# Kernel optimization log

Hardware: AMD Instinct MI355X
Metric: run time of the kernel (lower is better)

## Reference

```python
import jax, jax.numpy as jnp
import numpy as np

EPS = 0.1  # FAConv default eps


def setup_inputs() -> dict:
    key = jax.random.key(0)
    k1, k2, k3, k4, k5 = jax.random.split(key, 5)
    N, D, E, Dout = 50000, 128, 600000, 128
    x = jax.random.normal(k1, (N, D), dtype=jnp.float32)
    edge_index = jax.random.randint(k2, (2, E), 0, N, dtype=jnp.int64)
    # glorot-style scale for att vectors (Linear(D,1)) and weight matrix
    att_l = jax.random.normal(k3, (D,), dtype=jnp.float32) * (1.0 / np.sqrt(D))
    att_r = jax.random.normal(k4, (D,), dtype=jnp.float32) * (1.0 / np.sqrt(D))
    weight = jax.random.normal(k5, (D, Dout), dtype=jnp.float32) * np.sqrt(6.0 / (D + Dout))
    bias = jnp.zeros((Dout,), dtype=jnp.float32)
    return {"x": x, "edge_index": edge_index, "att_l": att_l, "att_r": att_r,
            "weight": weight, "bias": bias}


def reference(x, edge_index, att_l, att_r, weight, bias):
    N, D = x.shape
    # gcn_norm with add_self_loops=True
    loops = jnp.arange(N, dtype=edge_index.dtype)
    row = jnp.concatenate([edge_index[0], loops])  # source nodes
    col = jnp.concatenate([edge_index[1], loops])  # target nodes
    deg = jax.ops.segment_sum(jnp.ones_like(col, dtype=x.dtype), col, num_segments=N)
    dinv = jnp.where(deg > 0, jax.lax.rsqrt(jnp.maximum(deg, 1e-12)), 0.0)
    norm = dinv[row] * dinv[col]  # [E+N]
    # FAConv attention: alpha = tanh(att_l . x_j + att_r . x_i)
    al = x @ att_l  # [N]
    ar = x @ att_r  # [N]
    a = jnp.tanh(al[row] + ar[col])  # per-edge
    msg = x[row] * (a * norm)[:, None]  # [E+N, D]
    agg = jax.ops.segment_sum(msg, col, num_segments=N)
    h = agg + EPS * x  # x_0 == x in SAGNN.forward
    return h @ weight + bias
```

## Files before the change

kernel.cpp:

```cpp
#include <hip/hip_runtime.h>
#include <hip/hip_bf16.h>

#define FA_EPS 0.1f
#define BUCKET_M 48

typedef _Float16 half8  __attribute__((ext_vector_type(8)));
typedef float    f32x4  __attribute__((ext_vector_type(4)));

__device__ __forceinline__ float fast_tanh(float x) {
    float z = __builtin_amdgcn_exp2f(x * 2.885390081777927f);
    return 1.f - 2.f * __builtin_amdgcn_rcpf(z + 1.f);
}


__global__ __launch_bounds__(256) void k_node_prep(
    const float* __restrict__ x,
    const float* __restrict__ att_l,
    const float* __restrict__ att_r,
    const float* __restrict__ w,
    uint4* __restrict__ R,
    unsigned char* __restrict__ x8,
    _Float16* __restrict__ wt, int N)
{
    int gtid = (int)(blockIdx.x * blockDim.x + threadIdx.x);
    if (gtid < 128 * 128) {
        int k = gtid >> 7, n = gtid & 127;
        wt[n * 128 + k] = (_Float16)w[k * 128 + n];
    }
    int wave = gtid >> 6;
    int lane = threadIdx.x & 63;
    int half = lane >> 5;
    int sl   = lane & 31;
    int node = wave * 2 + half;
    if (node >= N) return;
    float4 v  = ((const float4*)(x + (size_t)node * 128))[sl];
    float4 l4 = ((const float4*)att_l)[sl];
    float4 r4 = ((const float4*)att_r)[sl];
    float pal = v.x * l4.x + v.y * l4.y + v.z * l4.z + v.w * l4.w;
    float par = v.x * r4.x + v.y * r4.y + v.z * r4.z + v.w * r4.w;
    float pm  = fmaxf(fmaxf(fabsf(v.x), fabsf(v.y)),
                      fmaxf(fabsf(v.z), fabsf(v.w)));
    #pragma unroll
    for (int off = 16; off > 0; off >>= 1) {
        pal += __shfl_xor(pal, off);
        par += __shfl_xor(par, off);
        pm   = fmaxf(pm, __shfl_xor(pm, off));
    }
    float rs = pm > 1e-20f ? 127.f / pm : 0.f;
    unsigned int q0 = (unsigned int)(int)rintf(fmaf(v.x, rs, 128.f));
    unsigned int q1 = (unsigned int)(int)rintf(fmaf(v.y, rs, 128.f));
    unsigned int q2 = (unsigned int)(int)rintf(fmaf(v.z, rs, 128.f));
    unsigned int q3 = (unsigned int)(int)rintf(fmaf(v.w, rs, 128.f));
    q0 = q0 > 255u ? 255u : q0;  q1 = q1 > 255u ? 255u : q1;
    q2 = q2 > 255u ? 255u : q2;  q3 = q3 > 255u ? 255u : q3;
    ((unsigned int*)(x8 + (size_t)node * 128))[sl] =
        q0 | (q1 << 8) | (q2 << 16) | (q3 << 24);
    if (sl == 0)
        R[node] = make_uint4(0u, __float_as_uint(pal),
                             __float_as_uint(pm * (1.f / 127.f)),
                             __float_as_uint(par));
}

__global__ __launch_bounds__(256) void k_edge(
    const int* __restrict__ ei,
    uint4* __restrict__ R,
    unsigned int* __restrict__ csr, int E)
{
    int e = (int)(blockIdx.x * blockDim.x + threadIdx.x);
    if (e >= E) return;
    int s = ei[e];
    int t = ei[E + e];
    unsigned int pos = atomicAdd((unsigned int*)(R + t), 1u);
    if (pos < BUCKET_M)
        csr[(size_t)t * BUCKET_M + pos] = (unsigned int)s;
}

__global__ __launch_bounds__(256) void k_gather(
    const unsigned char* __restrict__ x8,
    const unsigned int* __restrict__ csr,
    const uint4* __restrict__ R,
    _Float16* __restrict__ h16, int N)
{
    int wave = (int)((blockIdx.x * blockDim.x + threadIdx.x) >> 6);
    int lane = threadIdx.x & 63;
    int g  = lane >> 4;
    int sl = lane & 15;
    int t  = wave * 4 + g;
    bool valid = t < N;
    int tc = valid ? t : N - 1;
    uint4 rt = R[tc];
    unsigned int dt = rt.x;
    float al_t = __uint_as_float(rt.y);
    float s_t  = __uint_as_float(rt.z);
    float ar_t = __uint_as_float(rt.w);
    unsigned int cnt = dt < BUCKET_M ? dt : BUCKET_M;
    if (!valid) cnt = 0u;
    float dinv_t = __builtin_amdgcn_rsqf((float)(dt + 1u));
    const unsigned int* cs = csr + (size_t)tc * BUCKET_M;
    float acc[8];
    #pragma unroll
    for (int c = 0; c < 8; ++c) acc[c] = 0.f;
    float accB = 0.f;
    int gbase = lane & 0x30;
    for (unsigned int j0 = 0; j0 < cnt; j0 += 16) {
        unsigned int nb = cnt - j0; if (nb > 16u) nb = 16u;
        unsigned int myidx = j0 + (unsigned int)sl;
        bool own = myidx < cnt;
        unsigned int em = cs[own ? myidx : cnt - 1u];
        uint4 rsm = R[em];
        float am = own ? fast_tanh(__uint_as_float(rsm.y) + ar_t)
                         * __builtin_amdgcn_rsqf((float)(rsm.x + 1u))
                         * __uint_as_float(rsm.z)
                       : 0.f;
        const uint4* bp = (const uint4*)(cs + j0);
        uint4 b0 = bp[0], b1 = bp[1], b2 = bp[2], b3 = bp[3];
        unsigned int eu[16];
        eu[0]=b0.x;  eu[1]=b0.y;  eu[2]=b0.z;  eu[3]=b0.w;
        eu[4]=b1.x;  eu[5]=b1.y;  eu[6]=b1.z;  eu[7]=b1.w;
        eu[8]=b2.x;  eu[9]=b2.y;  eu[10]=b2.z; eu[11]=b2.w;
        eu[12]=b3.x; eu[13]=b3.y; eu[14]=b3.z; eu[15]=b3.w;
        uint2 d[16];
        #pragma unroll
        for (int u = 0; u < 16; ++u) {
            unsigned int e = (u < (int)nb) ? eu[u] : 0u;
            d[u] = *(const uint2*)(x8 + (size_t)e * 128 + sl * 8);
        }
        #pragma unroll
        for (int u = 0; u < 16; ++u) {
            float a = __shfl(am, gbase + u);
            accB += a;
            unsigned int lo = d[u].x, hi = d[u].y;
            acc[0] += a * (float)( lo        & 0xffu);
            acc[1] += a * (float)((lo >>  8) & 0xffu);
            acc[2] += a * (float)((lo >> 16) & 0xffu);
            acc[3] += a * (float)( lo >> 24        );
            acc[4] += a * (float)( hi        & 0xffu);
            acc[5] += a * (float)((hi >>  8) & 0xffu);
            acc[6] += a * (float)((hi >> 16) & 0xffu);
            acc[7] += a * (float)( hi >> 24        );
        }
    }
    float selfc  = fast_tanh(al_t + ar_t) * dinv_t * dinv_t + FA_EPS;
    float selfAs = selfc * s_t;
    float K = -128.f * fmaf(accB, dinv_t, selfAs);
    uint2 dself = *(const uint2*)(x8 + (size_t)tc * 128 + sl * 8);
    float bt[8];
    bt[0] = (float)( dself.x        & 0xffu);
    bt[1] = (float)((dself.x >>  8) & 0xffu);
    bt[2] = (float)((dself.x >> 16) & 0xffu);
    bt[3] = (float)( dself.x >> 24        );
    bt[4] = (float)( dself.y        & 0xffu);
    bt[5] = (float)((dself.y >>  8) & 0xffu);
    bt[6] = (float)((dself.y >> 16) & 0xffu);
    bt[7] = (float)( dself.y >> 24        );
    if (valid) {
        half8 hv;
        #pragma unroll
        for (int c = 0; c < 8; ++c)
            hv[c] = (_Float16)fmaf(acc[c], dinv_t, fmaf(selfAs, bt[c], K));
        *((half8*)(h16 + (size_t)t * 128) + sl) = hv;
    }
}

__global__ __launch_bounds__(256) void k_matmul_mfma(
    const _Float16* __restrict__ h16,
    const _Float16* __restrict__ wt,
    const float* __restrict__ bias,
    float* __restrict__ out, int N)
{
    __shared__ _Float16 wl[128 * 136];
    int tid = threadIdx.x;
    {
        const float* wsrc = (const float*)wt;
        float* wdst = (float*)wl;
        #pragma unroll
        for (int i = tid; i < 8192; i += 256)
            wdst[(i >> 6) * 68 + (i & 63)] = wsrc[i];
    }
    __syncthreads();
    int wv   = tid >> 6;
    int lane = tid & 63;
    int m    = lane & 15;
    int quad = lane >> 4;
    int r0 = (int)blockIdx.x * 64 + wv * 16;
    f32x4 acc[8];
    #pragma unroll
    for (int t = 0; t < 8; ++t) acc[t] = (f32x4)0.f;
    const _Float16* arow = h16 + (size_t)(r0 + m) * 128 + quad * 8;
    #pragma unroll
    for (int k0 = 0; k0 < 128; k0 += 32) {
        half8 a = *(const half8*)(arow + k0);
        #pragma unroll
        for (int t = 0; t < 8; ++t) {
            const _Float16* bp = wl + (size_t)(t * 16 + m) * 136 + quad * 8 + k0;
            half8 b = *(const half8*)bp;
            acc[t] = __builtin_amdgcn_mfma_f32_16x16x32_f16(a, b, acc[t], 0, 0, 0);
        }
    }
    int orow = r0 + quad * 4;
    #pragma unroll
    for (int t = 0; t < 8; ++t) {
        int col = t * 16 + m;
        float bc = bias[col];
        #pragma unroll
        for (int rg = 0; rg < 4; ++rg) {
            int r = orow + rg;
            if (r < N) out[(size_t)r * 128 + col] = acc[t][rg] + bc;
        }
    }
}

extern "C" void kernel_launch(void* const* d_in, const int* in_sizes, int n_in,
                              void* d_out, int out_size, void* d_ws, size_t ws_size,
                              hipStream_t stream)
{
    const float* x     = (const float*)d_in[0];
    const int*   ei    = (const int*)d_in[1];
    const float* att_l = (const float*)d_in[2];
    const float* att_r = (const float*)d_in[3];
    const float* w     = (const float*)d_in[4];
    const float* bias  = (const float*)d_in[5];
    float* out = (float*)d_out;

    const int N  = in_sizes[0] / 128;
    const int E  = in_sizes[1] / 2;
    const int NP = ((N + 63) / 64) * 64;

    char* ws = (char*)d_ws;
    _Float16*      h16 = (_Float16*)ws;
    unsigned char* x8  = (unsigned char*)(h16 + (size_t)NP * 128);
    uint4*         R   = (uint4*)(x8 + (size_t)N * 128);
    unsigned int*  csr = (unsigned int*)(R + N);
    _Float16*      wt  = (_Float16*)(csr + (size_t)N * BUCKET_M);

    {
        int waves = (N + 1) / 2;
        k_node_prep<<<(waves * 64 + 255) / 256, 256, 0, stream>>>(
            x, att_l, att_r, w, R, x8, wt, N);
    }
    k_edge<<<(E + 255) / 256, 256, 0, stream>>>(ei, R, csr, E);
    {
        int waves = (N + 3) / 4;
        k_gather<<<(waves * 64 + 255) / 256, 256, 0, stream>>>(
            x8, csr, R, h16, N);
    }
    k_matmul_mfma<<<NP / 64, 256, 0, stream>>>(h16, wt, bias, out, N);
}
```

Before: 147.0 us.

## Pad degree counters to separate lines and precompute per-node gather coefficients

```diff
diff --git a/kernel.cpp b/kernel.cpp
--- a/kernel.cpp
+++ b/kernel.cpp
@@ -18,7 +18,8 @@
     const float* __restrict__ att_l,
     const float* __restrict__ att_r,
     const float* __restrict__ w,
-    uint4* __restrict__ R,
+    uint4* __restrict__ A,
+    unsigned int* __restrict__ cur,
     unsigned char* __restrict__ x8,
     _Float16* __restrict__ wt, int N)
 {
@@ -55,30 +56,51 @@
     q2 = q2 > 255u ? 255u : q2;  q3 = q3 > 255u ? 255u : q3;
     ((unsigned int*)(x8 + (size_t)node * 128))[sl] =
         q0 | (q1 << 8) | (q2 << 16) | (q3 << 24);
-    if (sl == 0)
-        R[node] = make_uint4(0u, __float_as_uint(pal),
-                             __float_as_uint(pm * (1.f / 127.f)),
-                             __float_as_uint(par));
+    if (sl == 0) {
+        A[node] = make_uint4(__float_as_uint(pal), __float_as_uint(par),
+                             __float_as_uint(pm * (1.f / 127.f)), 0u);
+        cur[(size_t)node << 4] = 0u;
+    }
 }
 
 __global__ __launch_bounds__(256) void k_edge(
     const int* __restrict__ ei,
-    uint4* __restrict__ R,
+    unsigned int* __restrict__ cur,
     unsigned int* __restrict__ csr, int E)
 {
     int e = (int)(blockIdx.x * blockDim.x + threadIdx.x);
     if (e >= E) return;
     int s = ei[e];
     int t = ei[E + e];
-    unsigned int pos = atomicAdd((unsigned int*)(R + t), 1u);
+    unsigned int pos = atomicAdd(cur + ((size_t)t << 4), 1u);
     if (pos < BUCKET_M)
         csr[(size_t)t * BUCKET_M + pos] = (unsigned int)s;
+}
+
+__global__ __launch_bounds__(256) void k_finalize(
+    const unsigned int* __restrict__ cur,
+    uint4* __restrict__ A,
+    uint2* __restrict__ R2, int N)
+{
+    int n = (int)(blockIdx.x * blockDim.x + threadIdx.x);
+    if (n >= N) return;
+    unsigned int deg = cur[(size_t)n << 4];
+    uint4 a = A[n];
+    float al = __uint_as_float(a.x);
+    float ar = __uint_as_float(a.y);
+    float s  = __uint_as_float(a.z);
+    float dinv = __builtin_amdgcn_rsqf((float)(deg + 1u));
+    float selfAs = (fast_tanh(al + ar) * dinv * dinv + FA_EPS) * s;
+    R2[n] = make_uint2(__float_as_uint(al), __float_as_uint(dinv * s));
+    A[n]  = make_uint4(deg, __float_as_uint(dinv), __float_as_uint(ar),
+                       __float_as_uint(selfAs));
 }
 
 __global__ __launch_bounds__(256) void k_gather(
     const unsigned char* __restrict__ x8,
     const unsigned int* __restrict__ csr,
-    const uint4* __restrict__ R,
+    const uint4* __restrict__ T,
+    const uint2* __restrict__ R2,
     _Float16* __restrict__ h16, int N)
 {
     int wave = (int)((blockIdx.x * blockDim.x + threadIdx.x) >> 6);
@@ -88,14 +110,13 @@
     int t  = wave * 4 + g;
     bool valid = t < N;
     int tc = valid ? t : N - 1;
-    uint4 rt = R[tc];
-    unsigned int dt = rt.x;
-    float al_t = __uint_as_float(rt.y);
-    float s_t  = __uint_as_float(rt.z);
-    float ar_t = __uint_as_float(rt.w);
+    uint4 tt = T[tc];
+    unsigned int dt = tt.x;
+    float dinv_t  = __uint_as_float(tt.y);
+    float ar_t    = __uint_as_float(tt.z);
+    float selfAs  = __uint_as_float(tt.w);
     unsigned int cnt = dt < BUCKET_M ? dt : BUCKET_M;
     if (!valid) cnt = 0u;
-    float dinv_t = __builtin_amdgcn_rsqf((float)(dt + 1u));
     const unsigned int* cs = csr + (size_t)tc * BUCKET_M;
     float acc[8];
     #pragma unroll
@@ -107,10 +128,9 @@
         unsigned int myidx = j0 + (unsigned int)sl;
         bool own = myidx < cnt;
         unsigned int em = cs[own ? myidx : cnt - 1u];
-        uint4 rsm = R[em];
-        float am = own ? fast_tanh(__uint_as_float(rsm.y) + ar_t)
-                         * __builtin_amdgcn_rsqf((float)(rsm.x + 1u))
-                         * __uint_as_float(rsm.z)
+        uint2 rsm = R2[em];
+        float am = own ? fast_tanh(__uint_as_float(rsm.x) + ar_t)
+                         * __uint_as_float(rsm.y)
                        : 0.f;
         const uint4* bp = (const uint4*)(cs + j0);
         uint4 b0 = bp[0], b1 = bp[1], b2 = bp[2], b3 = bp[3];
@@ -140,8 +160,6 @@
             acc[7] += a * (float)( hi >> 24        );
         }
     }
-    float selfc  = fast_tanh(al_t + ar_t) * dinv_t * dinv_t + FA_EPS;
-    float selfAs = selfc * s_t;
     float K = -128.f * fmaf(accB, dinv_t, selfAs);
     uint2 dself = *(const uint2*)(x8 + (size_t)tc * 128 + sl * 8);
     float bt[8];
@@ -229,20 +247,23 @@
     char* ws = (char*)d_ws;
     _Float16*      h16 = (_Float16*)ws;
     unsigned char* x8  = (unsigned char*)(h16 + (size_t)NP * 128);
-    uint4*         R   = (uint4*)(x8 + (size_t)N * 128);
-    unsigned int*  csr = (unsigned int*)(R + N);
+    uint4*         A   = (uint4*)(x8 + (size_t)N * 128);
+    uint2*         R2  = (uint2*)(A + N);
+    unsigned int*  cur = (unsigned int*)(R2 + N);
+    unsigned int*  csr = cur + (size_t)N * 16;
     _Float16*      wt  = (_Float16*)(csr + (size_t)N * BUCKET_M);
 
     {
         int waves = (N + 1) / 2;
         k_node_prep<<<(waves * 64 + 255) / 256, 256, 0, stream>>>(
-            x, att_l, att_r, w, R, x8, wt, N);
-    }
-    k_edge<<<(E + 255) / 256, 256, 0, stream>>>(ei, R, csr, E);
+            x, att_l, att_r, w, A, cur, x8, wt, N);
+    }
+    k_edge<<<(E + 255) / 256, 256, 0, stream>>>(ei, cur, csr, E);
+    k_finalize<<<(N + 255) / 256, 256, 0, stream>>>(cur, A, R2, N);
     {
         int waves = (N + 3) / 4;
         k_gather<<<(waves * 64 + 255) / 256, 256, 0, stream>>>(
-            x8, csr, R, h16, N);
+            x8, csr, A, R2, h16, N);
     }
     k_matmul_mfma<<<NP / 64, 256, 0, stream>>>(h16, wt, bias, out, N);
 }
```

Result: no change. 149.8 us (+1.9%).

## Split gather feature loop into two halves and vectorize edge index loads

Applied to the files above, without the earlier changes.

```diff
diff --git a/kernel.cpp b/kernel.cpp
--- a/kernel.cpp
+++ b/kernel.cpp
@@ -5,6 +5,7 @@
 #define BUCKET_M 48
 
 typedef _Float16 half8  __attribute__((ext_vector_type(8)));
+typedef _Float16 half4v __attribute__((ext_vector_type(4)));
 typedef float    f32x4  __attribute__((ext_vector_type(4)));
 
 __device__ __forceinline__ float fast_tanh(float x) {
@@ -66,13 +67,18 @@
     uint4* __restrict__ R,
     unsigned int* __restrict__ csr, int E)
 {
-    int e = (int)(blockIdx.x * blockDim.x + threadIdx.x);
+    int e = (int)(blockIdx.x * blockDim.x + threadIdx.x) * 2;
     if (e >= E) return;
-    int s = ei[e];
-    int t = ei[E + e];
-    unsigned int pos = atomicAdd((unsigned int*)(R + t), 1u);
-    if (pos < BUCKET_M)
-        csr[(size_t)t * BUCKET_M + pos] = (unsigned int)s;
+    int2 ss = *(const int2*)(ei + e);
+    int2 tt = *(const int2*)(ei + E + e);
+    unsigned int p0 = atomicAdd((unsigned int*)(R + tt.x), 1u);
+    if (p0 < BUCKET_M)
+        csr[(size_t)tt.x * BUCKET_M + p0] = (unsigned int)ss.x;
+    if (e + 1 < E) {
+        unsigned int p1 = atomicAdd((unsigned int*)(R + tt.y), 1u);
+        if (p1 < BUCKET_M)
+            csr[(size_t)tt.y * BUCKET_M + p1] = (unsigned int)ss.y;
+    }
 }
 
 __global__ __launch_bounds__(256) void k_gather(
@@ -96,69 +102,64 @@
     unsigned int cnt = dt < BUCKET_M ? dt : BUCKET_M;
     if (!valid) cnt = 0u;
     float dinv_t = __builtin_amdgcn_rsqf((float)(dt + 1u));
+    float selfAs = (fast_tanh(al_t + ar_t) * dinv_t * dinv_t + FA_EPS) * s_t;
     const unsigned int* cs = csr + (size_t)tc * BUCKET_M;
-    float acc[8];
-    #pragma unroll
-    for (int c = 0; c < 8; ++c) acc[c] = 0.f;
-    float accB = 0.f;
     int gbase = lane & 0x30;
-    for (unsigned int j0 = 0; j0 < cnt; j0 += 16) {
-        unsigned int nb = cnt - j0; if (nb > 16u) nb = 16u;
-        unsigned int myidx = j0 + (unsigned int)sl;
-        bool own = myidx < cnt;
-        unsigned int em = cs[own ? myidx : cnt - 1u];
-        uint4 rsm = R[em];
-        float am = own ? fast_tanh(__uint_as_float(rsm.y) + ar_t)
-                         * __builtin_amdgcn_rsqf((float)(rsm.x + 1u))
-                         * __uint_as_float(rsm.z)
-                       : 0.f;
-        const uint4* bp = (const uint4*)(cs + j0);
-        uint4 b0 = bp[0], b1 = bp[1], b2 = bp[2], b3 = bp[3];
-        unsigned int eu[16];
-        eu[0]=b0.x;  eu[1]=b0.y;  eu[2]=b0.z;  eu[3]=b0.w;
-        eu[4]=b1.x;  eu[5]=b1.y;  eu[6]=b1.z;  eu[7]=b1.w;
-        eu[8]=b2.x;  eu[9]=b2.y;  eu[10]=b2.z; eu[11]=b2.w;
-        eu[12]=b3.x; eu[13]=b3.y; eu[14]=b3.z; eu[15]=b3.w;
-        uint2 d[16];
-        #pragma unroll
-        for (int u = 0; u < 16; ++u) {
-            unsigned int e = (u < (int)nb) ? eu[u] : 0u;
-            d[u] = *(const uint2*)(x8 + (size_t)e * 128 + sl * 8);
-        }
-        #pragma unroll
-        for (int u = 0; u < 16; ++u) {
-            float a = __shfl(am, gbase + u);
-            accB += a;
-            unsigned int lo = d[u].x, hi = d[u].y;
-            acc[0] += a * (float)( lo        & 0xffu);
-            acc[1] += a * (float)((lo >>  8) & 0xffu);
-            acc[2] += a * (float)((lo >> 16) & 0xffu);
-            acc[3] += a * (float)( lo >> 24        );
-            acc[4] += a * (float)( hi        & 0xffu);
-            acc[5] += a * (float)((hi >>  8) & 0xffu);
-            acc[6] += a * (float)((hi >> 16) & 0xffu);
-            acc[7] += a * (float)( hi >> 24        );
-        }
-    }
-    float selfc  = fast_tanh(al_t + ar_t) * dinv_t * dinv_t + FA_EPS;
-    float selfAs = selfc * s_t;
-    float K = -128.f * fmaf(accB, dinv_t, selfAs);
-    uint2 dself = *(const uint2*)(x8 + (size_t)tc * 128 + sl * 8);
-    float bt[8];
-    bt[0] = (float)( dself.x        & 0xffu);
-    bt[1] = (float)((dself.x >>  8) & 0xffu);
-    bt[2] = (float)((dself.x >> 16) & 0xffu);
-    bt[3] = (float)( dself.x >> 24        );
-    bt[4] = (float)( dself.y        & 0xffu);
-    bt[5] = (float)((dself.y >>  8) & 0xffu);
-    bt[6] = (float)((dself.y >> 16) & 0xffu);
-    bt[7] = (float)( dself.y >> 24        );
-    if (valid) {
-        half8 hv;
-        #pragma unroll
-        for (int c = 0; c < 8; ++c)
-            hv[c] = (_Float16)fmaf(acc[c], dinv_t, fmaf(selfAs, bt[c], K));
-        *((half8*)(h16 + (size_t)t * 128) + sl) = hv;
+
+    for (int p = 0; p < 2; ++p) {
+        float acc[4];
+        acc[0] = acc[1] = acc[2] = acc[3] = 0.f;
+        float accB = 0.f;
+        for (unsigned int j0 = 0; j0 < cnt; j0 += 16) {
+            unsigned int nb = cnt - j0; if (nb > 16u) nb = 16u;
+            unsigned int myidx = j0 + (unsigned int)sl;
+            bool own = myidx < cnt;
+            unsigned int em = cs[own ? myidx : cnt - 1u];
+            uint4 rsm = R[em];
+            float am = own ? fast_tanh(__uint_as_float(rsm.y) + ar_t)
+                             * __builtin_amdgcn_rsqf((float)(rsm.x + 1u))
+                             * __uint_as_float(rsm.z)
+                           : 0.f;
+            const uint4* bp = (const uint4*)(cs + j0);
+            uint4 b0 = bp[0], b1 = bp[1], b2 = bp[2], b3 = bp[3];
+            unsigned int eu[16];
+            eu[0]=b0.x;  eu[1]=b0.y;  eu[2]=b0.z;  eu[3]=b0.w;
+            eu[4]=b1.x;  eu[5]=b1.y;  eu[6]=b1.z;  eu[7]=b1.w;
+            eu[8]=b2.x;  eu[9]=b2.y;  eu[10]=b2.z; eu[11]=b2.w;
+            eu[12]=b3.x; eu[13]=b3.y; eu[14]=b3.z; eu[15]=b3.w;
+            unsigned int d[16];
+            #pragma unroll
+            for (int u = 0; u < 16; ++u) {
+                unsigned int e = (u < (int)nb) ? eu[u] : 0u;
+                d[u] = *(const unsigned int*)(x8 + (size_t)e * 128
+                                              + p * 64 + sl * 4);
+            }
+            #pragma unroll
+            for (int u = 0; u < 16; ++u) {
+                float a = __shfl(am, gbase + u);
+                accB += a;
+                unsigned int dd = d[u];
+                acc[0] += a * (float)( dd        & 0xffu);
+                acc[1] += a * (float)((dd >>  8) & 0xffu);
+                acc[2] += a * (float)((dd >> 16) & 0xffu);
+                acc[3] += a * (float)( dd >> 24        );
+            }
+        }
+        float K = -128.f * fmaf(accB, dinv_t, selfAs);
+        unsigned int dself = *(const unsigned int*)(x8 + (size_t)tc * 128
+                                                    + p * 64 + sl * 4);
+        if (valid) {
+            half4v hv;
+            hv[0] = (_Float16)fmaf(acc[0], dinv_t,
+                     fmaf(selfAs, (float)( dself        & 0xffu), K));
+            hv[1] = (_Float16)fmaf(acc[1], dinv_t,
+                     fmaf(selfAs, (float)((dself >>  8) & 0xffu), K));
+            hv[2] = (_Float16)fmaf(acc[2], dinv_t,
+                     fmaf(selfAs, (float)((dself >> 16) & 0xffu), K));
+            hv[3] = (_Float16)fmaf(acc[3], dinv_t,
+                     fmaf(selfAs, (float)( dself >> 24        ), K));
+            *(half4v*)(h16 + (size_t)t * 128 + p * 64 + sl * 4) = hv;
+        }
     }
 }
 
@@ -238,7 +239,7 @@
         k_node_prep<<<(waves * 64 + 255) / 256, 256, 0, stream>>>(
             x, att_l, att_r, w, R, x8, wt, N);
     }
-    k_edge<<<(E + 255) / 256, 256, 0, stream>>>(ei, R, csr, E);
+    k_edge<<<((E + 1) / 2 + 255) / 256, 256, 0, stream>>>(ei, R, csr, E);
     {
         int waves = (N + 3) / 4;
         k_gather<<<(waves * 64 + 255) / 256, 256, 0, stream>>>(
```

Measured after the change: 154.9 us. 1.05x slower.
